# Performance work log

Hardware: AMD Instinct MI355X
Metric: run time of the kernel (lower is better)

Reference implementation:

```python
import jax, jax.numpy as jnp
import numpy as np

KH, KW, PAD = 7, 7, 3  # 7x7 window, 'same' padding, stride 1


def setup_inputs() -> dict:
    key = jax.random.key(0)
    ks = jax.random.split(key, 7)
    b, c, h, w = 4, 256, 32, 32
    fc = 256
    rel_size = fc // 2
    ws = 1.0 / np.sqrt(c)
    rb = 1.0 / np.sqrt(rel_size)
    x = jax.random.normal(ks[0], (b, c, h, w), dtype=jnp.float32)
    Wq = jax.random.normal(ks[1], (c, fc), dtype=jnp.float32) * ws
    Wk = jax.random.normal(ks[2], (c, fc), dtype=jnp.float32) * ws
    Wv = jax.random.normal(ks[3], (c, fc), dtype=jnp.float32) * ws
    rel_x = jax.random.uniform(ks[4], (KW, rel_size), minval=-rb, maxval=rb, dtype=jnp.float32)
    rel_y = jax.random.uniform(ks[5], (KH, fc - rel_size), minval=-rb, maxval=rb, dtype=jnp.float32)
    bias = jax.random.uniform(ks[6], (fc,), minval=-1.0 / np.sqrt(fc), maxval=1.0 / np.sqrt(fc), dtype=jnp.float32)
    return {"x": x, "Wq": Wq, "Wk": Wk, "Wv": Wv, "rel_x": rel_x, "rel_y": rel_y, "bias": bias}


def _windows(t, kh, kw, pad):
    # t: (b, f, h, w) -> (b, f, kh*kw, h, w); stride-1 'same' window extraction
    b, f, h, w = t.shape
    tp = jnp.pad(t, ((0, 0), (0, 0), (pad, pad), (pad, pad)))
    return jnp.stack([tp[:, :, i:i + h, j:j + w] for i in range(kh) for j in range(kw)], axis=2)


def reference(x, Wq, Wk, Wv, rel_x, rel_y, bias):
    fc = Wq.shape[1]
    # per-pixel 1x1 projections (equivalent to projecting unfolded windows)
    q = jnp.einsum('bchw,cf->bfhw', x, Wq)  # center-pixel query
    k = jnp.einsum('bchw,cf->bfhw', x, Wk)
    v = jnp.einsum('bchw,cf->bfhw', x, Wv)
    kwin = _windows(k, KH, KW, PAD)  # (b, fc, K, h, w)
    vwin = _windows(v, KH, KW, PAD)
    # relative positional embedding: rel[ky, kx] = concat(rel_x[kx], rel_y[ky])
    rel = jnp.concatenate([
        jnp.broadcast_to(rel_x[None, :, :], (KH, KW, rel_x.shape[1])),
        jnp.broadcast_to(rel_y[:, None, :], (KH, KW, rel_y.shape[1])),
    ], axis=-1)  # (KH, KW, fc)
    rel = rel.reshape(KH * KW, fc).T[None, :, :, None, None]  # (1, fc, K, 1, 1)
    # per-channel score q * (k + rel), softmax over the window axis
    ab = q[:, :, None, :, :] * (kwin + rel)  # (b, fc, K, h, w)
    attn = jax.nn.softmax(ab, axis=2)
    out = (attn * vwin).sum(axis=2) + bias[None, :, None, None]
    return out
```

## Files before the change

kernel.cpp:

```cpp
#include <hip/hip_runtime.h>
#include <math.h>

#define C   256
#define FC  256
#define H   32
#define W   32
#define HW  1024
#define KH  7
#define KW  7
#define PAD 3
#define KK  49

typedef short s16x8 __attribute__((ext_vector_type(8)));
typedef float f32x4 __attribute__((ext_vector_type(4)));

__device__ __forceinline__ ushort f2bf(float f) {
    uint u = __float_as_uint(f);
    u += 0x7FFFu + ((u >> 16) & 1u);
    return (ushort)(u >> 16);
}
__device__ __forceinline__ float bf2f(ushort u) {
    return __uint_as_float(((uint)u) << 16);
}
__device__ __forceinline__ s16x8 pack8(const float* v) {
    s16x8 r;
    #pragma unroll
    for (int j = 0; j < 8; ++j) r[j] = (short)f2bf(v[j]);
    return r;
}

__global__ __launch_bounds__(256) void qkv_direct_kernel(
    const float* __restrict__ x,  const float* __restrict__ Wq,
    const float* __restrict__ Wk, const float* __restrict__ Wv,
    ushort* __restrict__ qo, ushort* __restrict__ ko, ushort* __restrict__ vo)
{
    const int t   = threadIdx.x;
    const int pxt = blockIdx.x;
    const int fg  = blockIdx.y;
    const int b   = blockIdx.z;

    const int wid = t >> 6, lane = t & 63;
    const int wf = wid >> 1, wp = wid & 1;
    const int lr = lane & 15;
    const int g  = lane >> 4;
    const int fbase = fg * 32 + wf * 16;
    const int px0   = pxt * 64 + wp * 32 + lr;

    const float* wqp = Wq + (size_t)(g * 8) * FC + fbase + lr;
    const float* wkp = Wk + (size_t)(g * 8) * FC + fbase + lr;
    const float* wvp = Wv + (size_t)(g * 8) * FC + fbase + lr;
    const float* xp0 = x + ((size_t)b * C + g * 8) * HW + px0;
    const float* xp1 = xp0 + 16;

    f32x4 acc00 = {0.f,0.f,0.f,0.f}, acc01 = {0.f,0.f,0.f,0.f};
    f32x4 acc10 = {0.f,0.f,0.f,0.f}, acc11 = {0.f,0.f,0.f,0.f};
    f32x4 acc20 = {0.f,0.f,0.f,0.f}, acc21 = {0.f,0.f,0.f,0.f};

    #pragma unroll
    for (int kk = 0; kk < 8; ++kk) {
        const int co = kk * 32;
        float aq[8], ak[8], av[8], b0[8], b1[8];
        #pragma unroll
        for (int j = 0; j < 8; ++j) {
            aq[j] = wqp[(size_t)(co + j) * FC];
            ak[j] = wkp[(size_t)(co + j) * FC];
            av[j] = wvp[(size_t)(co + j) * FC];
            b0[j] = xp0[(size_t)(co + j) * HW];
            b1[j] = xp1[(size_t)(co + j) * HW];
        }
        s16x8 A0 = pack8(aq), A1 = pack8(ak), A2 = pack8(av);
        s16x8 B0 = pack8(b0), B1 = pack8(b1);
        acc00 = __builtin_amdgcn_mfma_f32_16x16x32_bf16(A0, B0, acc00, 0, 0, 0);
        acc01 = __builtin_amdgcn_mfma_f32_16x16x32_bf16(A0, B1, acc01, 0, 0, 0);
        acc10 = __builtin_amdgcn_mfma_f32_16x16x32_bf16(A1, B0, acc10, 0, 0, 0);
        acc11 = __builtin_amdgcn_mfma_f32_16x16x32_bf16(A1, B1, acc11, 0, 0, 0);
        acc20 = __builtin_amdgcn_mfma_f32_16x16x32_bf16(A2, B0, acc20, 0, 0, 0);
        acc21 = __builtin_amdgcn_mfma_f32_16x16x32_bf16(A2, B1, acc21, 0, 0, 0);
    }

    const int fg4 = g * 4;
    #pragma unroll
    for (int j = 0; j < 4; ++j) {
        size_t ro = ((size_t)(b * FC + fbase + fg4 + j)) * HW + px0;
        qo[ro]      = f2bf(acc00[j]);
        qo[ro + 16] = f2bf(acc01[j]);
        ko[ro]      = f2bf(acc10[j]);
        ko[ro + 16] = f2bf(acc11[j]);
        vo[ro]      = f2bf(acc20[j]);
        vo[ro + 16] = f2bf(acc21[j]);
    }
}

__global__ __launch_bounds__(256) void attn_kernel(
    const ushort* __restrict__ q, const ushort* __restrict__ k,
    const ushort* __restrict__ v,
    const float* __restrict__ rel_x, const float* __restrict__ rel_y,
    const float* __restrict__ bias, float* __restrict__ out)
{
    __shared__ float ks[22][22];
    __shared__ float vs[22][22];
    __shared__ float rel_s[KK];

    const int b   = blockIdx.z;
    const int f   = blockIdx.y;
    const int th0 = (blockIdx.x >> 1) * 16;
    const int tw0 = (blockIdx.x & 1) * 16;
    const int tid = threadIdx.x;
    const int tx  = tid & 15;
    const int ty  = tid >> 4;

    if (tid < KK) {
        int dy = tid / KW, dx = tid % KW;
        rel_s[tid] = (f < 128) ? rel_x[dx * 128 + f]
                               : rel_y[dy * 128 + (f - 128)];
    }

    const ushort* kb = k + ((size_t)b * FC + f) * HW;
    const ushort* vb = v + ((size_t)b * FC + f) * HW;
    for (int i = tid; i < 22 * 22; i += 256) {
        int r = i / 22, c2 = i % 22;
        int hh = th0 - PAD + r;
        int ww = tw0 - PAD + c2;
        bool in = (hh >= 0) & (hh < H) & (ww >= 0) & (ww < W);
        ks[r][c2] = in ? bf2f(kb[hh * W + ww]) : 0.f;
        vs[r][c2] = in ? bf2f(vb[hh * W + ww]) : 0.f;
    }
    __syncthreads();

    const int hh = th0 + ty, ww = tw0 + tx;
    const float qv = bf2f(q[((size_t)b * FC + f) * HW + hh * W + ww]);

    float tt[KK];
    float m = -INFINITY;
    #pragma unroll
    for (int ki = 0; ki < KK; ++ki) {
        int dy = ki / KW, dx = ki % KW;
        float s = qv * (ks[ty + dy][tx + dx] + rel_s[ki]);
        tt[ki] = s;
        m = fmaxf(m, s);
    }

    float sum = 0.f, acc = 0.f;
    #pragma unroll
    for (int ki = 0; ki < KK; ++ki) {
        int dy = ki / KW, dx = ki % KW;
        float e = __expf(tt[ki] - m);
        sum += e;
        acc = fmaf(e, vs[ty + dy][tx + dx], acc);
    }

    out[((size_t)b * FC + f) * HW + hh * W + ww] = acc / sum + bias[f];
}

extern "C" void kernel_launch(void* const* d_in, const int* in_sizes, int n_in,
                              void* d_out, int out_size, void* d_ws, size_t ws_size,
                              hipStream_t stream)
{
    const float* x     = (const float*)d_in[0];
    const float* Wq    = (const float*)d_in[1];
    const float* Wk    = (const float*)d_in[2];
    const float* Wv    = (const float*)d_in[3];
    const float* rel_x = (const float*)d_in[4];
    const float* rel_y = (const float*)d_in[5];
    const float* bias  = (const float*)d_in[6];
    float* out = (float*)d_out;

    ushort* q  = (ushort*)d_ws;
    ushort* kk = q  + (size_t)4 * FC * HW;
    ushort* vv = kk + (size_t)4 * FC * HW;

    qkv_direct_kernel<<<dim3(16, 8, 4), 256, 0, stream>>>(x, Wq, Wk, Wv, q, kk, vv);
    attn_kernel<<<dim3(4, FC, 4), 256, 0, stream>>>(q, kk, vv, rel_x, rel_y, bias, out);
}
```

Measured before the change: 32.29 us.

## Store QKV channel-last and process eight channels per attention block

The projection kernel swaps MFMA operand order so it writes q/k/v in pixel-major, channel-last layout. The attention kernel then loads eight contiguous channels per pixel with 16-byte vector loads and handles eight channels per block, cutting the grid from 4096 to 512 blocks. This amortizes halo loads and rel/bias setup across channels, but each block does eight times more serial work, uses larger shared memory with possible bank conflicts from the [pos][8] stride, and has fewer blocks to spread across CUs.

New measurement: 42.80 us. 32.6% more time.

```diff
diff --git a/kernel.cpp b/kernel.cpp
--- a/kernel.cpp
+++ b/kernel.cpp
@@ -52,9 +52,9 @@
     const float* xp0 = x + ((size_t)b * C + g * 8) * HW + px0;
     const float* xp1 = xp0 + 16;
 
-    f32x4 acc00 = {0.f,0.f,0.f,0.f}, acc01 = {0.f,0.f,0.f,0.f};
-    f32x4 acc10 = {0.f,0.f,0.f,0.f}, acc11 = {0.f,0.f,0.f,0.f};
-    f32x4 acc20 = {0.f,0.f,0.f,0.f}, acc21 = {0.f,0.f,0.f,0.f};
+    f32x4 accq0 = {0.f,0.f,0.f,0.f}, accq1 = {0.f,0.f,0.f,0.f};
+    f32x4 acck0 = {0.f,0.f,0.f,0.f}, acck1 = {0.f,0.f,0.f,0.f};
+    f32x4 accv0 = {0.f,0.f,0.f,0.f}, accv1 = {0.f,0.f,0.f,0.f};
 
     #pragma unroll
     for (int kk = 0; kk < 8; ++kk) {
@@ -68,26 +68,24 @@
             b0[j] = xp0[(size_t)(co + j) * HW];
             b1[j] = xp1[(size_t)(co + j) * HW];
         }
-        s16x8 A0 = pack8(aq), A1 = pack8(ak), A2 = pack8(av);
-        s16x8 B0 = pack8(b0), B1 = pack8(b1);
-        acc00 = __builtin_amdgcn_mfma_f32_16x16x32_bf16(A0, B0, acc00, 0, 0, 0);
-        acc01 = __builtin_amdgcn_mfma_f32_16x16x32_bf16(A0, B1, acc01, 0, 0, 0);
-        acc10 = __builtin_amdgcn_mfma_f32_16x16x32_bf16(A1, B0, acc10, 0, 0, 0);
-        acc11 = __builtin_amdgcn_mfma_f32_16x16x32_bf16(A1, B1, acc11, 0, 0, 0);
-        acc20 = __builtin_amdgcn_mfma_f32_16x16x32_bf16(A2, B0, acc20, 0, 0, 0);
-        acc21 = __builtin_amdgcn_mfma_f32_16x16x32_bf16(A2, B1, acc21, 0, 0, 0);
+        s16x8 X0 = pack8(b0), X1 = pack8(b1);
+        s16x8 WQ = pack8(aq), WK = pack8(ak), WV = pack8(av);
+        accq0 = __builtin_amdgcn_mfma_f32_16x16x32_bf16(X0, WQ, accq0, 0, 0, 0);
+        accq1 = __builtin_amdgcn_mfma_f32_16x16x32_bf16(X1, WQ, accq1, 0, 0, 0);
+        acck0 = __builtin_amdgcn_mfma_f32_16x16x32_bf16(X0, WK, acck0, 0, 0, 0);
+        acck1 = __builtin_amdgcn_mfma_f32_16x16x32_bf16(X1, WK, acck1, 0, 0, 0);
+        accv0 = __builtin_amdgcn_mfma_f32_16x16x32_bf16(X0, WV, accv0, 0, 0, 0);
+        accv1 = __builtin_amdgcn_mfma_f32_16x16x32_bf16(X1, WV, accv1, 0, 0, 0);
     }
 
-    const int fg4 = g * 4;
     #pragma unroll
     for (int j = 0; j < 4; ++j) {
-        size_t ro = ((size_t)(b * FC + fbase + fg4 + j)) * HW + px0;
-        qo[ro]      = f2bf(acc00[j]);
-        qo[ro + 16] = f2bf(acc01[j]);
-        ko[ro]      = f2bf(acc10[j]);
-        ko[ro + 16] = f2bf(acc11[j]);
-        vo[ro]      = f2bf(acc20[j]);
-        vo[ro + 16] = f2bf(acc21[j]);
+        int pxr = pxt * 64 + wp * 32 + g * 4 + j;
+        size_t a0 = ((size_t)(b * HW) + pxr) * FC + fbase + lr;
+        size_t a1 = a0 + (size_t)16 * FC;
+        qo[a0] = f2bf(accq0[j]);  qo[a1] = f2bf(accq1[j]);
+        ko[a0] = f2bf(acck0[j]);  ko[a1] = f2bf(acck1[j]);
+        vo[a0] = f2bf(accv0[j]);  vo[a1] = f2bf(accv1[j]);
     }
 }
 
@@ -97,59 +95,79 @@
     const float* __restrict__ rel_x, const float* __restrict__ rel_y,
     const float* __restrict__ bias, float* __restrict__ out)
 {
-    __shared__ float ks[22][22];
-    __shared__ float vs[22][22];
-    __shared__ float rel_s[KK];
+    __shared__ float ks[484][8];
+    __shared__ float vs[484][8];
+    __shared__ float rel_s[KK][8];
+    __shared__ float bias_s[8];
 
-    const int b   = blockIdx.z;
-    const int f   = blockIdx.y;
-    const int th0 = (blockIdx.x >> 1) * 16;
-    const int tw0 = (blockIdx.x & 1) * 16;
-    const int tid = threadIdx.x;
-    const int tx  = tid & 15;
-    const int ty  = tid >> 4;
+    const int b    = blockIdx.z;
+    const int fg   = blockIdx.y;
+    const int tile = blockIdx.x;
+    const int f0   = fg * 8;
+    const int th0  = (tile >> 1) * 16;
+    const int tw0  = (tile & 1) * 16;
+    const int tid  = threadIdx.x;
+    const int tx   = tid & 15;
+    const int ty   = tid >> 4;
 
-    if (tid < KK) {
-        int dy = tid / KW, dx = tid % KW;
-        rel_s[tid] = (f < 128) ? rel_x[dx * 128 + f]
-                               : rel_y[dy * 128 + (f - 128)];
+    for (int i = tid; i < KK * 8; i += 256) {
+        int ki = i >> 3, fi = i & 7;
+        int dy = ki / KW, dx = ki % KW;
+        int f = f0 + fi;
+        rel_s[ki][fi] = (f < 128) ? rel_x[dx * 128 + f]
+                                  : rel_y[dy * 128 + (f - 128)];
     }
+    if (tid < 8) bias_s[tid] = bias[f0 + tid];
 
-    const ushort* kb = k + ((size_t)b * FC + f) * HW;
-    const ushort* vb = v + ((size_t)b * FC + f) * HW;
-    for (int i = tid; i < 22 * 22; i += 256) {
+    for (int i = tid; i < 484; i += 256) {
         int r = i / 22, c2 = i % 22;
         int hh = th0 - PAD + r;
         int ww = tw0 - PAD + c2;
         bool in = (hh >= 0) & (hh < H) & (ww >= 0) & (ww < W);
-        ks[r][c2] = in ? bf2f(kb[hh * W + ww]) : 0.f;
-        vs[r][c2] = in ? bf2f(vb[hh * W + ww]) : 0.f;
+        s16x8 k8 = {0,0,0,0,0,0,0,0}, v8 = {0,0,0,0,0,0,0,0};
+        if (in) {
+            size_t off = ((size_t)(b * HW) + hh * W + ww) * FC + f0;
+            k8 = *(const s16x8*)&k[off];
+            v8 = *(const s16x8*)&v[off];
+        }
+        #pragma unroll
+        for (int j = 0; j < 8; ++j) {
+            ks[i][j] = bf2f((ushort)k8[j]);
+            vs[i][j] = bf2f((ushort)v8[j]);
+        }
     }
     __syncthreads();
 
-    const int hh = th0 + ty, ww = tw0 + tx;
-    const float qv = bf2f(q[((size_t)b * FC + f) * HW + hh * W + ww]);
+    const int px = (th0 + ty) * W + tw0 + tx;
+    s16x8 q8 = *(const s16x8*)&q[((size_t)(b * HW) + px) * FC + f0];
+    float qs[8];
+    #pragma unroll
+    for (int j = 0; j < 8; ++j) qs[j] = bf2f((ushort)q8[j]);
 
-    float tt[KK];
-    float m = -INFINITY;
     #pragma unroll
-    for (int ki = 0; ki < KK; ++ki) {
-        int dy = ki / KW, dx = ki % KW;
-        float s = qv * (ks[ty + dy][tx + dx] + rel_s[ki]);
-        tt[ki] = s;
-        m = fmaxf(m, s);
+    for (int fi = 0; fi < 8; ++fi) {
+        const float qv = qs[fi];
+        float tt[KK];
+        float m = -INFINITY;
+        #pragma unroll
+        for (int ki = 0; ki < KK; ++ki) {
+            int dy = ki / KW, dx = ki % KW;
+            int pos = (ty + dy) * 22 + tx + dx;
+            float s = qv * (ks[pos][fi] + rel_s[ki][fi]);
+            tt[ki] = s;
+            m = fmaxf(m, s);
+        }
+        float sum = 0.f, acc = 0.f;
+        #pragma unroll
+        for (int ki = 0; ki < KK; ++ki) {
+            int dy = ki / KW, dx = ki % KW;
+            int pos = (ty + dy) * 22 + tx + dx;
+            float e = __expf(tt[ki] - m);
+            sum += e;
+            acc = fmaf(e, vs[pos][fi], acc);
+        }
+        out[((size_t)(b * FC) + f0 + fi) * HW + px] = acc / sum + bias_s[fi];
     }
-
-    float sum = 0.f, acc = 0.f;
-    #pragma unroll
-    for (int ki = 0; ki < KK; ++ki) {
-        int dy = ki / KW, dx = ki % KW;
-        float e = __expf(tt[ki] - m);
-        sum += e;
-        acc = fmaf(e, vs[ty + dy][tx + dx], acc);
-    }
-
-    out[((size_t)b * FC + f) * HW + hh * W + ww] = acc / sum + bias[f];
 }
 
 extern "C" void kernel_launch(void* const* d_in, const int* in_sizes, int n_in,
@@ -166,9 +184,9 @@
     float* out = (float*)d_out;
 
     ushort* q  = (ushort*)d_ws;
-    ushort* kk = q  + (size_t)4 * FC * HW;
-    ushort* vv = kk + (size_t)4 * FC * HW;
+    ushort* kk = q  + (size_t)4 * HW * FC;
+    ushort* vv = kk + (size_t)4 * HW * FC;
 
     qkv_direct_kernel<<<dim3(16, 8, 4), 256, 0, stream>>>(x, Wq, Wk, Wv, q, kk, vv);
-    attn_kernel<<<dim3(4, FC, 4), 256, 0, stream>>>(q, kk, vv, rel_x, rel_y, bias, out);
+    attn_kernel<<<dim3(4, 32, 4), 256, 0, stream>>>(q, kk, vv, rel_x, rel_y, bias, out);
 }
```
